# Performance work log

Hardware: AMD Instinct MI355X
Metric: run time of the kernel (lower is better)

Reference implementation:

```python
import jax, jax.numpy as jnp
import numpy as np

N, F, S, D = 8, 16, 196, 1024
H = 8
HD = D // H
L = 1 + F * S  # global feature token + f*s patch tokens


def _ln(x, g, b, eps=1e-5):
    m = x.mean(-1, keepdims=True)
    v = ((x - m) ** 2).mean(-1, keepdims=True)
    return (x - m) / jnp.sqrt(v + eps) * g + b


def _attn(q, k, v, hd):
    s = jnp.einsum('bqd,bkd->bqk', q, k) / jnp.sqrt(jnp.asarray(hd, q.dtype))
    return jnp.einsum('bqk,bkd->bqd', jax.nn.softmax(s, axis=-1), v)


def setup_inputs() -> dict:
    key = jax.random.key(0)
    ks = jax.random.split(key, 8)
    sc = 0.02
    return {
        'x': jax.random.normal(ks[0], (N, L, D), jnp.float32),
        'W_in': jax.random.normal(ks[1], (D, D), jnp.float32) * sc,
        'b_in': jnp.zeros((D,), jnp.float32),
        'g_in': jnp.ones((D,), jnp.float32),
        'beta_in': jnp.zeros((D,), jnp.float32),
        'W_q': jax.random.normal(ks[2], (D, D), jnp.float32) * sc,
        'W_k': jax.random.normal(ks[3], (D, D), jnp.float32) * sc,
        'W_v': jax.random.normal(ks[4], (D, D), jnp.float32) * sc,
        'g_out': jnp.ones((D,), jnp.float32),
        'beta_out': jnp.zeros((D,), jnp.float32),
        'W_out': jax.random.normal(ks[5], (D, D), jnp.float32) * sc,
        'b_out': jnp.zeros((D,), jnp.float32),
        'att_type': 1,  # 1 == 'time', 0 == 'space' (static)
    }


def reference(x, W_in, b_in, g_in, beta_in, W_q, W_k, W_v, g_out, beta_out, W_out, b_out, att_type):
    n = x.shape[0]
    nh = n * H
    # in_fc: Linear + LayerNorm
    x = _ln(x @ W_in + b_in, g_in, beta_in)
    q, k, v = x @ W_q, x @ W_k, x @ W_v

    def split_heads(y):  # [n, L, D] -> [n*h, L, hd]
        return y.reshape(n, L, H, HD).transpose(0, 2, 1, 3).reshape(nh, L, HD)

    q, k, v = map(split_heads, (q, k, v))
    feat_q, q = q[:, :1], q[:, 1:]
    feat_k, k = k[:, :1], k[:, 1:]
    feat_v, v = v[:, :1], v[:, 1:]

    # token_att is computed in the original but never used (dead code):
    # token_att = _attn(feat_q, k, v, HD)

    if att_type == 1:  # time attention: windows of length F per spatial site
        qt = q.reshape(nh, F, S, HD).transpose(0, 2, 1, 3).reshape(nh * S, F, HD)
        kt = k.reshape(nh, F, S, HD).transpose(0, 2, 1, 3).reshape(nh * S, F, HD)
        vt = v.reshape(nh, F, S, HD).transpose(0, 2, 1, 3).reshape(nh * S, F, HD)
        fk = jnp.tile(feat_k, (S, 1, 1))  # torch .repeat(s,1,1)
        fv = jnp.tile(feat_v, (S, 1, 1))
        kk = jnp.concatenate((fk, kt), axis=1)  # [nh*s, 1+f, hd]
        vv = jnp.concatenate((fv, vt), axis=1)
        seq = _attn(qt, kk, vv, HD)  # [nh*s, f, hd]
        seq = seq.reshape(nh, S, F, HD).transpose(0, 2, 1, 3).reshape(nh, F * S, HD)
    else:  # space attention: windows of length S per frame
        qs = q.reshape(nh * F, S, HD)
        ks_ = k.reshape(nh * F, S, HD)
        vs = v.reshape(nh * F, S, HD)
        fk = jnp.tile(feat_k, (F, 1, 1))
        fv = jnp.tile(feat_v, (F, 1, 1))
        kk = jnp.concatenate((fk, ks_), axis=1)  # [nh*f, 1+s, hd]
        vv = jnp.concatenate((fv, vs), axis=1)
        seq = _attn(qs, kk, vv, HD)  # [nh*f, s, hd]
        seq = seq.reshape(nh, F * S, HD)

    out = jnp.concatenate((feat_q, seq), axis=1)  # [nh, L, hd]
    out = out.reshape(n, H, L, HD).transpose(0, 2, 1, 3).reshape(n, L, D)
    out = _ln(out, g_out, beta_out) @ W_out + b_out
    return out
```

## Files before the change

### kernel.cpp

```cpp
#include <hip/hip_runtime.h>
#include <stdint.h>

#define N_B 8
#define F_T 16
#define S_T 196
#define D_M 1024
#define H_N 8
#define HD  128
#define L_T 3137
#define M_R (N_B * L_T)
#define M_P 25216

typedef __attribute__((ext_vector_type(8))) short bf16x8;
typedef __attribute__((ext_vector_type(4))) float f32x4;

__device__ __forceinline__ float b2f(unsigned int u) {
  union { unsigned int i; float f; } x; x.i = u << 16; return x.f;
}
__device__ __forceinline__ unsigned short f2b(float f) {
  union { float f; unsigned int i; } x; x.f = f;
  unsigned int r = x.i + 0x7fffu + ((x.i >> 16) & 1u);
  return (unsigned short)(r >> 16);
}

__global__ __launch_bounds__(256) void convert_pad(const float* __restrict__ x,
                                                   unsigned short* __restrict__ xb,
                                                   int nreal) {
  const int total4 = M_P * 1024 / 4;
  const int stride = gridDim.x * 256;
  for (int i = blockIdx.x * 256 + threadIdx.x; i < total4; i += stride) {
    const int e = i * 4;
    float4 v;
    if (e < nreal) v = *(const float4*)(x + e);
    else { v.x = 0.f; v.y = 0.f; v.z = 0.f; v.w = 0.f; }
    ushort4 o;
    o.x = f2b(v.x); o.y = f2b(v.y); o.z = f2b(v.z); o.w = f2b(v.w);
    *(ushort4*)(xb + e) = o;
  }
}

struct WP { const float* s[5]; unsigned short* d[5]; };
__global__ __launch_bounds__(256) void transpose5(WP p) {
  __shared__ float t[32][33];
  const int w = blockIdx.z;
  const float* W = p.s[w];
  unsigned short* Wt = p.d[w];
  const int tx = threadIdx.x, ty = threadIdx.y;
  const int n0 = blockIdx.x * 32, k0 = blockIdx.y * 32;
#pragma unroll
  for (int i = 0; i < 4; i++)
    t[ty + i * 8][tx] = W[(size_t)(k0 + ty + i * 8) * D_M + n0 + tx];
  __syncthreads();
#pragma unroll
  for (int i = 0; i < 4; i++)
    Wt[(size_t)(n0 + ty + i * 8) * D_M + k0 + tx] = f2b(t[tx][ty + i * 8]);
}

__device__ __forceinline__ void async16(const unsigned short* g, unsigned short* l) {
  __builtin_amdgcn_global_load_lds((const __attribute__((address_space(1))) void*)g,
                                   (__attribute__((address_space(3))) void*)l, 16, 0, 0);
}

struct Outs { void* p[3]; };

#define MFMA_Q(AV, MLO)                                                        \
  __builtin_amdgcn_s_setprio(1);                                               \
  _Pragma("unroll") for (int m_ = 0; m_ < 4; ++m_)                             \
      _Pragma("unroll") for (int n_ = 0; n_ < 4; ++n_)                         \
          acc[(MLO) + m_][n_] = __builtin_amdgcn_mfma_f32_16x16x32_bf16(       \
              AV[(MLO) + m_], bv[n_], acc[(MLO) + m_][n_], 0, 0, 0);           \
  __builtin_amdgcn_s_setprio(0);

#define TILE_ONE(T, BUF, STGB, STGA, VMN)                                      \
  do {                                                                         \
    const unsigned short* Ab = sA + (BUF) * 16384 + aOff;                      \
    const unsigned short* Bb = sB + (BUF) * 16384 + bOff;                      \
    if (STGB) {                                                                \
      async16(gB + ((T) + 1) * 64,          sBst + (1 - (BUF)) * 16384);       \
      async16(gB + ((T) + 1) * 64 + 65536,  sBst + (1 - (BUF)) * 16384 + 4096);\
    }                                                                          \
    _Pragma("unroll") for (int m_ = 0; m_ < 4; ++m_)                           \
        av0[m_] = *(const bf16x8*)(Ab + m_ * 1024 + sl0);                      \
    _Pragma("unroll") for (int n_ = 0; n_ < 4; ++n_)                           \
        bv[n_] = *(const bf16x8*)(Bb + n_ * 1024 + sl0);                       \
    _Pragma("unroll") for (int m_ = 0; m_ < 4; ++m_)                           \
        av1[m_] = *(const bf16x8*)(Ab + m_ * 1024 + sl1);                      \
    MFMA_Q(av0, 0)                                                             \
    if (STGB) {                                                                \
      async16(gB + ((T) + 1) * 64 + 131072, sBst + (1 - (BUF)) * 16384 + 8192);\
      async16(gB + ((T) + 1) * 64 + 196608, sBst + (1 - (BUF)) * 16384 + 12288);\
    }                                                                          \
    _Pragma("unroll") for (int m_ = 0; m_ < 4; ++m_)                           \
        av0[4 + m_] = *(const bf16x8*)(Ab + (4 + m_) * 1024 + sl0);            \
    _Pragma("unroll") for (int m_ = 0; m_ < 4; ++m_)                           \
        av1[4 + m_] = *(const bf16x8*)(Ab + (4 + m_) * 1024 + sl1);            \
    MFMA_Q(av0, 4)                                                             \
    asm volatile("s_waitcnt lgkmcnt(0)" ::: "memory");                         \
    __builtin_amdgcn_s_barrier();                                              \
    asm volatile("" ::: "memory");                                             \
    if (STGA) {                                                                \
      async16(gA + ((T) + 2) * 64,          sAst + (BUF) * 16384);             \
      async16(gA + ((T) + 2) * 64 + 65536,  sAst + (BUF) * 16384 + 4096);      \
    }                                                                          \
    _Pragma("unroll") for (int n_ = 0; n_ < 4; ++n_)                           \
        bv[n_] = *(const bf16x8*)(Bb + n_ * 1024 + sl1);                       \
    MFMA_Q(av1, 0)                                                             \
    if (STGA) {                                                                \
      async16(gA + ((T) + 2) * 64 + 131072, sAst + (BUF) * 16384 + 8192);      \
      async16(gA + ((T) + 2) * 64 + 196608, sAst + (BUF) * 16384 + 12288);     \
    }                                                                          \
    MFMA_Q(av1, 4)                                                             \
    if ((VMN) == 4)                                                            \
      asm volatile("s_waitcnt vmcnt(4) lgkmcnt(0)" ::: "memory");              \
    else if ((VMN) == 0)                                                       \
      asm volatile("s_waitcnt vmcnt(0) lgkmcnt(0)" ::: "memory");              \
    else                                                                       \
      asm volatile("s_waitcnt lgkmcnt(0)" ::: "memory");                       \
    __builtin_amdgcn_s_barrier();                                              \
    asm volatile("" ::: "memory");                                             \
  } while (0)

template <int MODE>
__global__ __launch_bounds__(512, 2) void gemm_bt(const unsigned short* __restrict__ A,
                                                  const unsigned short* __restrict__ Bt,
                                                  const float* __restrict__ bias,
                                                  Outs o, int Mreal) {
  __shared__ __align__(16) unsigned short lds[65536];
  unsigned short* sA = lds;
  unsigned short* sB = lds + 32768;

  const int tid = threadIdx.x;
  const int lane = tid & 63;
  const int wv = tid >> 6;
  const int wm = wv >> 2, wn = wv & 3;
  const int l15 = lane & 15, kg = lane >> 4;

  constexpr int NCT = (MODE == 3) ? 12 : 4;
  constexpr int NWG = 99 * NCT;
  constexpr int Q8 = NWG >> 3, R8 = NWG & 7;
  const int xcd = blockIdx.x & 7, off = blockIdx.x >> 3;
  const int lin = (xcd < R8 ? xcd * (Q8 + 1) : R8 * (Q8 + 1) + (xcd - R8) * Q8) + off;
  const int band = lin / 396;
  const int rem = lin - band * 396;
  const int rowBase = (rem >> 2) * 256;
  const int colBase = (band * 4 + (rem & 3)) * 256;

  const int srow = lane >> 3;
  const int gk = ((lane & 7) ^ srow) * 8;
  const unsigned short* gA = A + (size_t)(rowBase + wv * 8 + srow) * 1024 + gk;
  const unsigned short* gB = Bt + (size_t)(colBase + wv * 8 + srow) * 1024 + gk;
  unsigned short* sAst = sA + wv * 512 + lane * 8;
  unsigned short* sBst = sB + wv * 512 + lane * 8;

  const int aOff = (wm * 128 + l15) * 64;
  const int bOff = (wn * 64 + l15) * 64;
  const int sl0 = ((kg) ^ (l15 & 7)) * 8;
  const int sl1 = ((4 + kg) ^ (l15 & 7)) * 8;

  f32x4 acc[8][4] = {};
  bf16x8 av0[8], av1[8], bv[4];

#pragma unroll
  for (int i = 0; i < 4; i++) async16(gA + i * 65536, sAst + i * 4096);
#pragma unroll
  for (int i = 0; i < 4; i++) async16(gB + i * 65536, sBst + i * 4096);
#pragma unroll
  for (int i = 0; i < 4; i++) async16(gA + i * 65536 + 64, sAst + 16384 + i * 4096);
  asm volatile("s_waitcnt vmcnt(4)" ::: "memory");
  __builtin_amdgcn_s_barrier();
  asm volatile("" ::: "memory");

#pragma unroll 1
  for (int tp = 0; tp < 7; ++tp) {
    const int t0 = tp * 2;
    TILE_ONE(t0, 0, true, true, 4);
    TILE_ONE(t0 + 1, 1, true, true, 4);
  }
  TILE_ONE(14, 0, true, false, 0);
  TILE_ONE(15, 1, false, false, -1);

  __syncthreads();
  if (MODE == 2) {
    float* Cf = (float*)lds;
    float* outF = (float*)o.p[0];
#pragma unroll
    for (int p = 0; p < 2; ++p) {
      if (p) __syncthreads();
      if (wm == p) {
#pragma unroll
        for (int n = 0; n < 4; ++n) {
          const int col_l = wn * 64 + n * 16 + l15;
          const float bval = bias[colBase + col_l];
#pragma unroll
          for (int m = 0; m < 8; ++m)
#pragma unroll
            for (int r = 0; r < 4; ++r)
              Cf[(m * 16 + kg * 4 + r) * 256 + col_l] = acc[m][n][r] + bval;
        }
      }
      __syncthreads();
#pragma unroll
      for (int t2 = 0; t2 < 16; ++t2) {
        const int g = t2 * 512 + tid;
        const int row = g >> 6, ch = g & 63;
        const int grow = rowBase + p * 128 + row;
        if (grow < Mreal)
          *(float4*)(outF + (size_t)grow * 1024 + colBase + ch * 4) =
              *(const float4*)(Cf + row * 256 + ch * 4);
      }
    }
  } else {
    unsigned short* Cs = lds;
#pragma unroll
    for (int n = 0; n < 4; ++n) {
      const int col_l = wn * 64 + n * 16 + l15;
      const float bval = (MODE == 1) ? bias[colBase + col_l] : 0.f;
#pragma unroll
      for (int m = 0; m < 8; ++m)
#pragma unroll
        for (int r = 0; r < 4; ++r)
          Cs[(wm * 128 + m * 16 + kg * 4 + r) * 256 + col_l] = f2b(acc[m][n][r] + bval);
    }
    __syncthreads();
    unsigned short* C;
    int cbase;
    if (MODE == 3) { C = (unsigned short*)o.p[colBase >> 10]; cbase = colBase & 1023; }
    else { C = (unsigned short*)o.p[0]; cbase = colBase; }
#pragma unroll
    for (int t2 = 0; t2 < 16; ++t2) {
      const int g = t2 * 512 + tid;
      const int row = g >> 5, ch = g & 31;
      const int grow = rowBase + row;
      if (grow < Mreal)
        *(uint4*)(C + (size_t)grow * 1024 + cbase + ch * 8) =
            *(const uint4*)(Cs + row * 256 + ch * 8);
    }
  }
}

__global__ __launch_bounds__(256) void ln_kernel(const unsigned short* __restrict__ src,
                                                 const unsigned short* __restrict__ src0,
                                                 const float* __restrict__ g,
                                                 const float* __restrict__ beta,
                                                 unsigned short* __restrict__ out, int Mreal) {
  const int wv = threadIdx.x >> 6, lane = threadIdx.x & 63;
  const int row = blockIdx.x * 4 + wv;
  const int c0 = lane * 8;
  unsigned short* op = out + (size_t)row * 1024 + c0;
  if (row >= Mreal) {
    uint4 z; z.x = 0; z.y = 0; z.z = 0; z.w = 0;
    *(uint4*)op = z; *(uint4*)(op + 512) = z;
    return;
  }
  const unsigned short* s = src;
  if (src0 != nullptr && (row % L_T) == 0) s = src0;
  const unsigned short* ip = s + (size_t)row * 1024 + c0;
  const uint4 ra = *(const uint4*)ip;
  const uint4 rb = *(const uint4*)(ip + 512);
  float xs[16];
  xs[0] = b2f(ra.x & 0xffffu);  xs[1] = b2f(ra.x >> 16);
  xs[2] = b2f(ra.y & 0xffffu);  xs[3] = b2f(ra.y >> 16);
  xs[4] = b2f(ra.z & 0xffffu);  xs[5] = b2f(ra.z >> 16);
  xs[6] = b2f(ra.w & 0xffffu);  xs[7] = b2f(ra.w >> 16);
  xs[8] = b2f(rb.x & 0xffffu);  xs[9] = b2f(rb.x >> 16);
  xs[10] = b2f(rb.y & 0xffffu); xs[11] = b2f(rb.y >> 16);
  xs[12] = b2f(rb.z & 0xffffu); xs[13] = b2f(rb.z >> 16);
  xs[14] = b2f(rb.w & 0xffffu); xs[15] = b2f(rb.w >> 16);
  float sum = 0.f, sq = 0.f;
#pragma unroll
  for (int i = 0; i < 16; ++i) { sum += xs[i]; sq += xs[i] * xs[i]; }
#pragma unroll
  for (int off = 32; off > 0; off >>= 1) {
    sum += __shfl_xor(sum, off);
    sq += __shfl_xor(sq, off);
  }
  const float mean = sum * (1.f / 1024.f);
  const float var = sq * (1.f / 1024.f) - mean * mean;
  const float rstd = rsqrtf(var + 1e-5f);
  const float4 g0 = *(const float4*)(g + c0),        g1 = *(const float4*)(g + c0 + 4);
  const float4 g2 = *(const float4*)(g + c0 + 512),  g3 = *(const float4*)(g + c0 + 516);
  const float4 b0 = *(const float4*)(beta + c0),       b1 = *(const float4*)(beta + c0 + 4);
  const float4 b2 = *(const float4*)(beta + c0 + 512), b3 = *(const float4*)(beta + c0 + 516);
  float gg[16] = {g0.x, g0.y, g0.z, g0.w, g1.x, g1.y, g1.z, g1.w,
                  g2.x, g2.y, g2.z, g2.w, g3.x, g3.y, g3.z, g3.w};
  float bb[16] = {b0.x, b0.y, b0.z, b0.w, b1.x, b1.y, b1.z, b1.w,
                  b2.x, b2.y, b2.z, b2.w, b3.x, b3.y, b3.z, b3.w};
  unsigned short ov[16];
#pragma unroll
  for (int i = 0; i < 16; ++i) ov[i] = f2b((xs[i] - mean) * rstd * gg[i] + bb[i]);
  uint4 wa, wb;
  wa.x = (unsigned)ov[0] | ((unsigned)ov[1] << 16);
  wa.y = (unsigned)ov[2] | ((unsigned)ov[3] << 16);
  wa.z = (unsigned)ov[4] | ((unsigned)ov[5] << 16);
  wa.w = (unsigned)ov[6] | ((unsigned)ov[7] << 16);
  wb.x = (unsigned)ov[8] | ((unsigned)ov[9] << 16);
  wb.y = (unsigned)ov[10] | ((unsigned)ov[11] << 16);
  wb.z = (unsigned)ov[12] | ((unsigned)ov[13] << 16);
  wb.w = (unsigned)ov[14] | ((unsigned)ov[15] << 16);
  *(uint4*)op = wa;
  *(uint4*)(op + 512) = wb;
}

#define ATT_T_BLOCKS (64 * 49)
__global__ __launch_bounds__(256) void attn_kernel(const unsigned short* __restrict__ q,
                                                   const unsigned short* __restrict__ k,
                                                   const unsigned short* __restrict__ v,
                                                   unsigned short* __restrict__ out,
                                                   const int* __restrict__ att_type) {
  __shared__ __align__(16) char smem[22528];
  const int tid = threadIdx.x;
  const int bid = blockIdx.x;
  const int at = att_type[0];

  if (at == 1) {
    if (bid >= ATT_T_BLOCKS) return;
    const int lane = tid & 63, wv = tid >> 6;
    const int l15 = lane & 15, kg = lane >> 4;
    const int hb = bid / 49, sb = bid - hb * 49;
    const int s = sb * 4 + wv;
    const int n = hb >> 3, h = hb & 7;
    const int fi = (hb * S_T + s) & 63;
    const size_t frow = (size_t)(fi >> 3) * L_T;
    const int fcol = (fi & 7) * HD;
    const int qbase = n * L_T + 1 + s;
    const int hcol = h * HD;

    unsigned short* Pl = (unsigned short*)(smem + wv * 5632);
    unsigned short* Vl = (unsigned short*)(smem + wv * 5632 + 1024);

    {
      const int dim0 = l15 * 8;
#pragma unroll
      for (int p = 0; p < 5; p++) {
        const int key = p * 4 + kg;
        if (key < 17) {
          const unsigned short* vp = (key == 0)
              ? (v + frow * 1024 + fcol + dim0)
              : (v + (size_t)(qbase + (key - 1) * S_T) * 1024 + hcol + dim0);
          uint4 r = *(const uint4*)vp;
          unsigned int* wp = (unsigned int*)Vl + key * 65 + l15 * 4;
          wp[0] = r.x; wp[1] = r.y; wp[2] = r.z; wp[3] = r.w;
        }
      }
    }

    bf16x8 aq[4], bk0[4], bk1[4];
    {
      const unsigned short* qp = q + (size_t)(qbase + l15 * S_T) * 1024 + hcol + kg * 8;
      const unsigned short* kp = (l15 == 0)
          ? (k + frow * 1024 + fcol + kg * 8)
          : (k + (size_t)(qbase + (l15 - 1) * S_T) * 1024 + hcol + kg * 8);
      const unsigned short* kp1 = k + (size_t)(qbase + 15 * S_T) * 1024 + hcol + kg * 8;
#pragma unroll
      for (int t = 0; t < 4; t++) {
        aq[t] = *(const bf16x8*)(qp + t * 32);
        bk0[t] = *(const bf16x8*)(kp + t * 32);
        if (l15 == 0) bk1[t] = *(const bf16x8*)(kp1 + t * 32);
        else {
          bf16x8 z = {};
          bk1[t] = z;
        }
      }
    }

    f32x4 c0 = {}, c1 = {};
#pragma unroll
    for (int t = 0; t < 4; t++) {
      c0 = __builtin_amdgcn_mfma_f32_16x16x32_bf16(aq[t], bk0[t], c0, 0, 0, 0);
      c1 = __builtin_amdgcn_mfma_f32_16x16x32_bf16(aq[t], bk1[t], c1, 0, 0, 0);
    }

    const float scl = 0.08838834764831845f;
#pragma unroll
    for (int r = 0; r < 4; r++) {
      float v0 = c0[r] * scl;
      float k16 = __shfl(c1[r] * scl, lane & 48);
      float mx = v0;
#pragma unroll
      for (int m = 1; m < 16; m <<= 1) mx = fmaxf(mx, __shfl_xor(mx, m));
      mx = fmaxf(mx, k16);
      float p = __expf(v0 - mx);
      float p16 = __expf(k16 - mx);
      float sum = p;
#pragma unroll
      for (int m = 1; m < 16; m <<= 1) sum += __shfl_xor(sum, m);
      sum += p16;
      const float inv = 1.f / sum;
      const int row = kg * 4 + r;
      Pl[row * 32 + l15] = f2b(p * inv);
      Pl[row * 32 + 16 + l15] = (l15 == 0) ? f2b(p16 * inv) : (unsigned short)0;
    }

    bf16x8 ap = *(const bf16x8*)(Pl + l15 * 32 + kg * 8);
    f32x4 oo[8];
#pragma unroll
    for (int nt = 0; nt < 8; nt++) {
      const int dim = nt * 16 + l15;
      bf16x8 bvv;
#pragma unroll
      for (int j = 0; j < 8; j++) {
        const int key = kg * 8 + j;
        const int kc = (key < 17) ? key : 0;
        bvv[j] = (short)Vl[kc * 130 + dim];
      }
      f32x4 z = {};
      oo[nt] = __builtin_amdgcn_mfma_f32_16x16x32_bf16(ap, bvv, z, 0, 0, 0);
    }

#pragma unroll
    for (int nt = 0; nt < 8; nt++)
#pragma unroll
      for (int r = 0; r < 4; r++)
        Vl[(kg * 4 + r) * 130 + nt * 16 + l15] = f2b(oo[nt][r]);
#pragma unroll
    for (int t = 0; t < 4; t++) {
      const int row = t * 4 + kg;
      uint4 w = *(const uint4*)(Vl + row * 130 + l15 * 8);
      *(uint4*)(out + (size_t)(qbase + row * S_T) * 1024 + hcol + l15 * 8) = w;
    }
    return;
  }

  float (*qs)[132] = (float (*)[132])smem;
  float (*sc)[212] = (float (*)[212])(smem + 8448);
  const int hb = bid / 208;
  const int rem = bid - hb * 208;
  const int f = rem / 13, qc = rem - f * 13;
  const int n = hb >> 3, h = hb & 7;
  const int fi = (hb * F_T + f) & 63;
  const size_t frow = (size_t)(fi >> 3) * L_T;
  const int fcol = (fi & 7) * HD;
  const int kbase = n * L_T + 1 + f * S_T;
  const int qbase = kbase + qc * 16;
  const int nk = S_T + 1;
  const int nqv = (qc == 12) ? 4 : 16;
  const int hcol = h * HD;

  {
    const int i = tid >> 4, db = (tid & 15) * 8;
    float* dst = &qs[i][db];
    if (i < nqv) {
      const unsigned short* qp = q + (size_t)(qbase + i) * 1024 + hcol + db;
      uint4 r = *(const uint4*)qp;
      dst[0] = b2f(r.x & 0xffffu); dst[1] = b2f(r.x >> 16);
      dst[2] = b2f(r.y & 0xffffu); dst[3] = b2f(r.y >> 16);
      dst[4] = b2f(r.z & 0xffffu); dst[5] = b2f(r.z >> 16);
      dst[6] = b2f(r.w & 0xffffu); dst[7] = b2f(r.w >> 16);
    } else {
#pragma unroll
      for (int u = 0; u < 8; u++) dst[u] = 0.f;
    }
  }
  __syncthreads();

  const int nslot = 16 * nk;
  for (int slot = tid; slot < nslot; slot += 256) {
    const int i = slot / nk, j = slot - i * nk;
    const unsigned short* kp = (j == 0)
        ? (k + frow * 1024 + fcol)
        : (k + (size_t)(kbase + (j - 1)) * 1024 + hcol);
    float acc = 0.f;
#pragma unroll 4
    for (int d = 0; d < 128; d += 8) {
      uint4 r = *(const uint4*)(kp + d);
      acc += qs[i][d + 0] * b2f(r.x & 0xffffu);
      acc += qs[i][d + 1] * b2f(r.x >> 16);
      acc += qs[i][d + 2] * b2f(r.y & 0xffffu);
      acc += qs[i][d + 3] * b2f(r.y >> 16);
      acc += qs[i][d + 4] * b2f(r.z & 0xffffu);
      acc += qs[i][d + 5] * b2f(r.z >> 16);
      acc += qs[i][d + 6] * b2f(r.w & 0xffffu);
      acc += qs[i][d + 7] * b2f(r.w >> 16);
    }
    sc[i][j] = acc * 0.08838834764831845f;
  }
  __syncthreads();

  if (tid < 16) {
    const int i = tid;
    float m = -1e30f;
    for (int j = 0; j < nk; j++) m = fmaxf(m, sc[i][j]);
    float ssum = 0.f;
    for (int j = 0; j < nk; j++) {
      float e = __expf(sc[i][j] - m);
      sc[i][j] = e;
      ssum += e;
    }
    const float inv = 1.f / ssum;
    for (int j = 0; j < nk; j++) sc[i][j] *= inv;
  }
  __syncthreads();

  {
    const int i = tid >> 4, db = (tid & 15) * 8;
    float o[8];
#pragma unroll
    for (int u = 0; u < 8; u++) o[u] = 0.f;
    for (int j = 0; j < nk; j++) {
      const unsigned short* vp = (j == 0)
          ? (v + frow * 1024 + fcol + db)
          : (v + (size_t)(kbase + (j - 1)) * 1024 + hcol + db);
      const float p = sc[i][j];
      uint4 r = *(const uint4*)vp;
      o[0] += p * b2f(r.x & 0xffffu); o[1] += p * b2f(r.x >> 16);
      o[2] += p * b2f(r.y & 0xffffu); o[3] += p * b2f(r.y >> 16);
      o[4] += p * b2f(r.z & 0xffffu); o[5] += p * b2f(r.z >> 16);
      o[6] += p * b2f(r.w & 0xffffu); o[7] += p * b2f(r.w >> 16);
    }
    if (i < nqv) {
      unsigned short* op = out + (size_t)(qbase + i) * 1024 + hcol + db;
      uint4 w;
      w.x = (unsigned)f2b(o[0]) | ((unsigned)f2b(o[1]) << 16);
      w.y = (unsigned)f2b(o[2]) | ((unsigned)f2b(o[3]) << 16);
      w.z = (unsigned)f2b(o[4]) | ((unsigned)f2b(o[5]) << 16);
      w.w = (unsigned)f2b(o[6]) | ((unsigned)f2b(o[7]) << 16);
      *(uint4*)op = w;
    }
  }
}

extern "C" void kernel_launch(void* const* d_in, const int* in_sizes, int n_in,
                              void* d_out, int out_size, void* d_ws, size_t ws_size,
                              hipStream_t stream) {
  const float* x        = (const float*)d_in[0];
  const float* W_in     = (const float*)d_in[1];
  const float* b_in     = (const float*)d_in[2];
  const float* g_in     = (const float*)d_in[3];
  const float* beta_in  = (const float*)d_in[4];
  const float* W_q      = (const float*)d_in[5];
  const float* W_k      = (const float*)d_in[6];
  const float* W_v      = (const float*)d_in[7];
  const float* g_out    = (const float*)d_in[8];
  const float* beta_out = (const float*)d_in[9];
  const float* W_out    = (const float*)d_in[10];
  const float* b_out    = (const float*)d_in[11];
  const int* att_type   = (const int*)d_in[12];
  float* out = (float*)d_out;

  char* ws = (char*)d_ws;
  const size_t MB = (size_t)M_P * 1024 * 2;
  unsigned short* xb = (unsigned short*)(ws + 0 * MB);
  unsigned short* t1 = (unsigned short*)(ws + 1 * MB);
  unsigned short* xh = (unsigned short*)(ws + 2 * MB);
  unsigned short* kb = (unsigned short*)(ws + 3 * MB);
  unsigned short* vb = (unsigned short*)(ws + 4 * MB);
  unsigned short* wt = (unsigned short*)(ws + 5 * MB);
  const size_t WSZ = (size_t)1024 * 1024;
  unsigned short* wt_in  = wt;
  unsigned short* wqkv   = wt + 1 * WSZ;
  unsigned short* wt_out = wt + 4 * WSZ;

  convert_pad<<<2048, 256, 0, stream>>>(x, xb, M_R * 1024);

  WP wp;
  wp.s[0] = W_in; wp.s[1] = W_q; wp.s[2] = W_k; wp.s[3] = W_v; wp.s[4] = W_out;
  wp.d[0] = wt_in;
  wp.d[1] = wqkv;
  wp.d[2] = wqkv + 1 * WSZ;
  wp.d[3] = wqkv + 2 * WSZ;
  wp.d[4] = wt_out;
  transpose5<<<dim3(32, 32, 5), dim3(32, 8), 0, stream>>>(wp);

  Outs o1; o1.p[0] = t1; o1.p[1] = nullptr; o1.p[2] = nullptr;
  gemm_bt<1><<<396, 512, 0, stream>>>(xb, wt_in, b_in, o1, M_P);
  ln_kernel<<<M_P / 4, 256, 0, stream>>>(t1, nullptr, g_in, beta_in, xh, M_R);

  Outs oq; oq.p[0] = t1; oq.p[1] = kb; oq.p[2] = vb;
  gemm_bt<3><<<1188, 512, 0, stream>>>(xh, wqkv, nullptr, oq, M_P);

  attn_kernel<<<13312, 256, 0, stream>>>(t1, kb, vb, xb, att_type);
  ln_kernel<<<M_P / 4, 256, 0, stream>>>(xb, t1, g_out, beta_out, xh, M_R);

  Outs oo; oo.p[0] = out; oo.p[1] = nullptr; oo.p[2] = nullptr;
  gemm_bt<2><<<396, 512, 0, stream>>>(xh, wt_out, b_out, oo, M_R);
}
```

Measured before the change: 548.7 us.

## Fold LayerNorms into GEMM epilogues via weight scaling and row statistics

Removes both standalone LayerNorm kernels. LayerNorm gamma is folded into the transposed weights, and precomputed column sums (u = g·W, w = beta·W) let the following GEMM apply mean/rstd correction in its epilogue. Row sum and sum-of-squares are accumulated with atomics in the producing GEMM or attention epilogues. This saves two full read/write passes over the activation, at the cost of atomics, an extra small stats kernel, and numerical risk from the E[x²]-mean² variance formula on un-normalized bf16 inputs.

```diff
diff --git a/kernel.cpp b/kernel.cpp
--- a/kernel.cpp
+++ b/kernel.cpp
@@ -10,6 +10,7 @@
 #define L_T 3137
 #define M_R (N_B * L_T)
 #define M_P 25216
+#define M_T 25344
 
 typedef __attribute__((ext_vector_type(8))) short bf16x8;
 typedef __attribute__((ext_vector_type(4))) float f32x4;
@@ -39,21 +40,56 @@
   }
 }
 
-struct WP { const float* s[5]; unsigned short* d[5]; };
+struct WP { const float* s[5]; unsigned short* d[5]; const float* g[5]; };
 __global__ __launch_bounds__(256) void transpose5(WP p) {
   __shared__ float t[32][33];
   const int w = blockIdx.z;
   const float* W = p.s[w];
   unsigned short* Wt = p.d[w];
+  const float* gsp = p.g[w];
   const int tx = threadIdx.x, ty = threadIdx.y;
   const int n0 = blockIdx.x * 32, k0 = blockIdx.y * 32;
 #pragma unroll
   for (int i = 0; i < 4; i++)
     t[ty + i * 8][tx] = W[(size_t)(k0 + ty + i * 8) * D_M + n0 + tx];
   __syncthreads();
+  const float gs = gsp ? gsp[k0 + tx] : 1.f;
 #pragma unroll
   for (int i = 0; i < 4; i++)
-    Wt[(size_t)(n0 + ty + i * 8) * D_M + k0 + tx] = f2b(t[tx][ty + i * 8]);
+    Wt[(size_t)(n0 + ty + i * 8) * D_M + k0 + tx] = f2b(t[tx][ty + i * 8] * gs);
+}
+
+__global__ __launch_bounds__(256) void ustats(const float* __restrict__ Wq,
+                                              const float* __restrict__ Wk,
+                                              const float* __restrict__ Wv,
+                                              const float* __restrict__ Wo,
+                                              const float* __restrict__ g_in,
+                                              const float* __restrict__ beta_in,
+                                              const float* __restrict__ g_out,
+                                              const float* __restrict__ beta_out,
+                                              const float* __restrict__ b_out,
+                                              float* __restrict__ uvec,
+                                              float* __restrict__ wvec) {
+  const int jb = blockIdx.x >> 4;
+  const int chunk = blockIdx.x & 15;
+  const int j = jb * 256 + threadIdx.x;
+  const float* W; const float* g; const float* be; int col;
+  if (j < 3072) {
+    const int wsel = j >> 10;
+    W = (wsel == 0) ? Wq : ((wsel == 1) ? Wk : Wv);
+    col = j & 1023; g = g_in; be = beta_in;
+  } else {
+    W = Wo; col = j - 3072; g = g_out; be = beta_out;
+  }
+  float au = 0.f, aw = 0.f;
+  const int k0 = chunk * 64;
+  for (int k = k0; k < k0 + 64; ++k) {
+    const float wv_ = W[(size_t)k * 1024 + col];
+    au += g[k] * wv_; aw += be[k] * wv_;
+  }
+  if (chunk == 0 && j >= 3072) aw += b_out[col];
+  atomicAdd(&uvec[j], au);
+  atomicAdd(&wvec[j], aw);
 }
 
 __device__ __forceinline__ void async16(const unsigned short* g, unsigned short* l) {
@@ -124,7 +160,11 @@
 __global__ __launch_bounds__(512, 2) void gemm_bt(const unsigned short* __restrict__ A,
                                                   const unsigned short* __restrict__ Bt,
                                                   const float* __restrict__ bias,
-                                                  Outs o, int Mreal) {
+                                                  Outs o, int Mreal,
+                                                  float* __restrict__ st1,
+                                                  float* __restrict__ st2,
+                                                  const float* __restrict__ uvec,
+                                                  const float* __restrict__ wvec) {
   __shared__ __align__(16) unsigned short lds[65536];
   unsigned short* sA = lds;
   unsigned short* sB = lds + 32768;
@@ -183,20 +223,30 @@
   if (MODE == 2) {
     float* Cf = (float*)lds;
     float* outF = (float*)o.p[0];
+    float uu[4], ww[4];
+#pragma unroll
+    for (int n = 0; n < 4; ++n) {
+      const int c = colBase + wn * 64 + n * 16 + l15;
+      uu[n] = uvec[c]; ww[n] = wvec[c];
+    }
 #pragma unroll
     for (int p = 0; p < 2; ++p) {
       if (p) __syncthreads();
       if (wm == p) {
 #pragma unroll
-        for (int n = 0; n < 4; ++n) {
-          const int col_l = wn * 64 + n * 16 + l15;
-          const float bval = bias[colBase + col_l];
-#pragma unroll
-          for (int m = 0; m < 8; ++m)
-#pragma unroll
-            for (int r = 0; r < 4; ++r)
-              Cf[(m * 16 + kg * 4 + r) * 256 + col_l] = acc[m][n][r] + bval;
-        }
+        for (int m = 0; m < 8; ++m)
+#pragma unroll
+          for (int r = 0; r < 4; ++r) {
+            const int lrow = m * 16 + kg * 4 + r;
+            const int grow = rowBase + p * 128 + lrow;
+            const float2 st = *(const float2*)(st2 + (size_t)grow * 2);
+            const float mu = st.x * (1.f / 1024.f);
+            const float rstd = rsqrtf(st.y * (1.f / 1024.f) - mu * mu + 1e-5f);
+#pragma unroll
+            for (int n = 0; n < 4; ++n)
+              Cf[lrow * 256 + wn * 64 + n * 16 + l15] =
+                  rstd * (acc[m][n][r] - mu * uu[n]) + ww[n];
+          }
       }
       __syncthreads();
 #pragma unroll
@@ -209,23 +259,86 @@
               *(const float4*)(Cf + row * 256 + ch * 4);
       }
     }
+  } else if (MODE == 1) {
+    unsigned short* Cs = lds;
+    float bvals[4];
+#pragma unroll
+    for (int n = 0; n < 4; ++n) bvals[n] = bias[colBase + wn * 64 + n * 16 + l15];
+#pragma unroll
+    for (int m = 0; m < 8; ++m)
+#pragma unroll
+      for (int r = 0; r < 4; ++r) {
+        const int lrow = wm * 128 + m * 16 + kg * 4 + r;
+        float s = 0.f, sq = 0.f;
+#pragma unroll
+        for (int n = 0; n < 4; ++n) {
+          const float v = acc[m][n][r] + bvals[n];
+          Cs[lrow * 256 + wn * 64 + n * 16 + l15] = f2b(v);
+          s += v; sq += v * v;
+        }
+        s += __shfl_xor(s, 1); sq += __shfl_xor(sq, 1);
+        s += __shfl_xor(s, 2); sq += __shfl_xor(sq, 2);
+        s += __shfl_xor(s, 4); sq += __shfl_xor(sq, 4);
+        s += __shfl_xor(s, 8); sq += __shfl_xor(sq, 8);
+        if (l15 == 0) {
+          const int grow = rowBase + lrow;
+          atomicAdd(&st1[(size_t)grow * 2], s);
+          atomicAdd(&st1[(size_t)grow * 2 + 1], sq);
+        }
+      }
+    __syncthreads();
+    unsigned short* C = (unsigned short*)o.p[0];
+#pragma unroll
+    for (int t2 = 0; t2 < 16; ++t2) {
+      const int g = t2 * 512 + tid;
+      const int row = g >> 5, ch = g & 31;
+      const int grow = rowBase + row;
+      if (grow < Mreal)
+        *(uint4*)(C + (size_t)grow * 1024 + colBase + ch * 8) =
+            *(const uint4*)(Cs + row * 256 + ch * 8);
+    }
   } else {
     unsigned short* Cs = lds;
+    float uu[4], ww[4];
 #pragma unroll
     for (int n = 0; n < 4; ++n) {
-      const int col_l = wn * 64 + n * 16 + l15;
-      const float bval = (MODE == 1) ? bias[colBase + col_l] : 0.f;
-#pragma unroll
-      for (int m = 0; m < 8; ++m)
-#pragma unroll
-        for (int r = 0; r < 4; ++r)
-          Cs[(wm * 128 + m * 16 + kg * 4 + r) * 256 + col_l] = f2b(acc[m][n][r] + bval);
-    }
+      const int c = colBase + wn * 64 + n * 16 + l15;
+      uu[n] = uvec[c]; ww[n] = wvec[c];
+    }
+    const int r0m = rowBase % L_T;
+    const int flocal = (r0m == 0) ? 0 : (L_T - r0m);
+    const bool qtile = (colBase < 1024);
+#pragma unroll
+    for (int m = 0; m < 8; ++m)
+#pragma unroll
+      for (int r = 0; r < 4; ++r) {
+        const int lrow = wm * 128 + m * 16 + kg * 4 + r;
+        const int grow = rowBase + lrow;
+        const float2 st = *(const float2*)(st1 + (size_t)grow * 2);
+        const float mu = st.x * (1.f / 1024.f);
+        const float rstd = rsqrtf(st.y * (1.f / 1024.f) - mu * mu + 1e-5f);
+        float vv[4];
+#pragma unroll
+        for (int n = 0; n < 4; ++n) {
+          vv[n] = rstd * (acc[m][n][r] - mu * uu[n]) + ww[n];
+          Cs[lrow * 256 + wn * 64 + n * 16 + l15] = f2b(vv[n]);
+        }
+        if (qtile && lrow == flocal) {
+          float s = vv[0] + vv[1] + vv[2] + vv[3];
+          float sq = vv[0] * vv[0] + vv[1] * vv[1] + vv[2] * vv[2] + vv[3] * vv[3];
+          s += __shfl_xor(s, 1); sq += __shfl_xor(sq, 1);
+          s += __shfl_xor(s, 2); sq += __shfl_xor(sq, 2);
+          s += __shfl_xor(s, 4); sq += __shfl_xor(sq, 4);
+          s += __shfl_xor(s, 8); sq += __shfl_xor(sq, 8);
+          if (l15 == 0) {
+            atomicAdd(&st2[(size_t)grow * 2], s);
+            atomicAdd(&st2[(size_t)grow * 2 + 1], sq);
+          }
+        }
+      }
     __syncthreads();
-    unsigned short* C;
-    int cbase;
-    if (MODE == 3) { C = (unsigned short*)o.p[colBase >> 10]; cbase = colBase & 1023; }
-    else { C = (unsigned short*)o.p[0]; cbase = colBase; }
+    unsigned short* C = (unsigned short*)o.p[colBase >> 10];
+    const int cbase = colBase & 1023;
 #pragma unroll
     for (int t2 = 0; t2 < 16; ++t2) {
       const int g = t2 * 512 + tid;
@@ -238,79 +351,22 @@
   }
 }
 
-__global__ __launch_bounds__(256) void ln_kernel(const unsigned short* __restrict__ src,
-                                                 const unsigned short* __restrict__ src0,
-                                                 const float* __restrict__ g,
-                                                 const float* __restrict__ beta,
-                                                 unsigned short* __restrict__ out, int Mreal) {
-  const int wv = threadIdx.x >> 6, lane = threadIdx.x & 63;
-  const int row = blockIdx.x * 4 + wv;
-  const int c0 = lane * 8;
-  unsigned short* op = out + (size_t)row * 1024 + c0;
-  if (row >= Mreal) {
-    uint4 z; z.x = 0; z.y = 0; z.z = 0; z.w = 0;
-    *(uint4*)op = z; *(uint4*)(op + 512) = z;
-    return;
-  }
-  const unsigned short* s = src;
-  if (src0 != nullptr && (row % L_T) == 0) s = src0;
-  const unsigned short* ip = s + (size_t)row * 1024 + c0;
-  const uint4 ra = *(const uint4*)ip;
-  const uint4 rb = *(const uint4*)(ip + 512);
-  float xs[16];
-  xs[0] = b2f(ra.x & 0xffffu);  xs[1] = b2f(ra.x >> 16);
-  xs[2] = b2f(ra.y & 0xffffu);  xs[3] = b2f(ra.y >> 16);
-  xs[4] = b2f(ra.z & 0xffffu);  xs[5] = b2f(ra.z >> 16);
-  xs[6] = b2f(ra.w & 0xffffu);  xs[7] = b2f(ra.w >> 16);
-  xs[8] = b2f(rb.x & 0xffffu);  xs[9] = b2f(rb.x >> 16);
-  xs[10] = b2f(rb.y & 0xffffu); xs[11] = b2f(rb.y >> 16);
-  xs[12] = b2f(rb.z & 0xffffu); xs[13] = b2f(rb.z >> 16);
-  xs[14] = b2f(rb.w & 0xffffu); xs[15] = b2f(rb.w >> 16);
-  float sum = 0.f, sq = 0.f;
-#pragma unroll
-  for (int i = 0; i < 16; ++i) { sum += xs[i]; sq += xs[i] * xs[i]; }
-#pragma unroll
-  for (int off = 32; off > 0; off >>= 1) {
-    sum += __shfl_xor(sum, off);
-    sq += __shfl_xor(sq, off);
-  }
-  const float mean = sum * (1.f / 1024.f);
-  const float var = sq * (1.f / 1024.f) - mean * mean;
-  const float rstd = rsqrtf(var + 1e-5f);
-  const float4 g0 = *(const float4*)(g + c0),        g1 = *(const float4*)(g + c0 + 4);
-  const float4 g2 = *(const float4*)(g + c0 + 512),  g3 = *(const float4*)(g + c0 + 516);
-  const float4 b0 = *(const float4*)(beta + c0),       b1 = *(const float4*)(beta + c0 + 4);
-  const float4 b2 = *(const float4*)(beta + c0 + 512), b3 = *(const float4*)(beta + c0 + 516);
-  float gg[16] = {g0.x, g0.y, g0.z, g0.w, g1.x, g1.y, g1.z, g1.w,
-                  g2.x, g2.y, g2.z, g2.w, g3.x, g3.y, g3.z, g3.w};
-  float bb[16] = {b0.x, b0.y, b0.z, b0.w, b1.x, b1.y, b1.z, b1.w,
-                  b2.x, b2.y, b2.z, b2.w, b3.x, b3.y, b3.z, b3.w};
-  unsigned short ov[16];
-#pragma unroll
-  for (int i = 0; i < 16; ++i) ov[i] = f2b((xs[i] - mean) * rstd * gg[i] + bb[i]);
-  uint4 wa, wb;
-  wa.x = (unsigned)ov[0] | ((unsigned)ov[1] << 16);
-  wa.y = (unsigned)ov[2] | ((unsigned)ov[3] << 16);
-  wa.z = (unsigned)ov[4] | ((unsigned)ov[5] << 16);
-  wa.w = (unsigned)ov[6] | ((unsigned)ov[7] << 16);
-  wb.x = (unsigned)ov[8] | ((unsigned)ov[9] << 16);
-  wb.y = (unsigned)ov[10] | ((unsigned)ov[11] << 16);
-  wb.z = (unsigned)ov[12] | ((unsigned)ov[13] << 16);
-  wb.w = (unsigned)ov[14] | ((unsigned)ov[15] << 16);
-  *(uint4*)op = wa;
-  *(uint4*)(op + 512) = wb;
-}
-
 #define ATT_T_BLOCKS (64 * 49)
 __global__ __launch_bounds__(256) void attn_kernel(const unsigned short* __restrict__ q,
                                                    const unsigned short* __restrict__ k,
                                                    const unsigned short* __restrict__ v,
                                                    unsigned short* __restrict__ out,
-                                                   const int* __restrict__ att_type) {
+                                                   const int* __restrict__ att_type,
+                                                   float* __restrict__ st2) {
   __shared__ __align__(16) char smem[22528];
   const int tid = threadIdx.x;
   const int bid = blockIdx.x;
   const int at = att_type[0];
+
+  if (bid < N_B) {
+    const size_t ro = (size_t)bid * L_T * 1024;
+    *(uint2*)(out + ro + tid * 4) = *(const uint2*)(q + ro + tid * 4);
+  }
 
   if (at == 1) {
     if (bid >= ATT_T_BLOCKS) return;
@@ -405,6 +461,22 @@
       }
       f32x4 z = {};
       oo[nt] = __builtin_amdgcn_mfma_f32_16x16x32_bf16(ap, bvv, z, 0, 0, 0);
+    }
+
+#pragma unroll
+    for (int r = 0; r < 4; r++) {
+      float s = 0.f, sq = 0.f;
+#pragma unroll
+      for (int nt = 0; nt < 8; nt++) { const float vv = oo[nt][r]; s += vv; sq += vv * vv; }
+      s += __shfl_xor(s, 1); sq += __shfl_xor(sq, 1);
+      s += __shfl_xor(s, 2); sq += __shfl_xor(sq, 2);
+      s += __shfl_xor(s, 4); sq += __shfl_xor(sq, 4);
+      s += __shfl_xor(s, 8); sq += __shfl_xor(sq, 8);
+      if (l15 == 0) {
+        const size_t grow = (size_t)(qbase + (kg * 4 + r) * S_T);
+        atomicAdd(&st2[grow * 2], s);
+        atomicAdd(&st2[grow * 2 + 1], sq);
+      }
     }
 
 #pragma unroll
@@ -516,6 +588,18 @@
       w.w = (unsigned)f2b(o[6]) | ((unsigned)f2b(o[7]) << 16);
       *(uint4*)op = w;
     }
+    float s = 0.f, sq = 0.f;
+#pragma unroll
+    for (int u = 0; u < 8; u++) { s += o[u]; sq += o[u] * o[u]; }
+    s += __shfl_xor(s, 1); sq += __shfl_xor(sq, 1);
+    s += __shfl_xor(s, 2); sq += __shfl_xor(sq, 2);
+    s += __shfl_xor(s, 4); sq += __shfl_xor(sq, 4);
+    s += __shfl_xor(s, 8); sq += __shfl_xor(sq, 8);
+    if ((tid & 15) == 0 && i < nqv) {
+      const size_t grow = (size_t)(qbase + i);
+      atomicAdd(&st2[grow * 2], s);
+      atomicAdd(&st2[grow * 2 + 1], sq);
+    }
   }
 }
 
@@ -549,6 +633,12 @@
   unsigned short* wt_in  = wt;
   unsigned short* wqkv   = wt + 1 * WSZ;
   unsigned short* wt_out = wt + 4 * WSZ;
+  float* stats1 = (float*)(ws + 5 * MB + 5 * WSZ * sizeof(unsigned short));
+  float* stats2 = stats1 + 2 * M_T;
+  float* uvec   = stats2 + 2 * M_T;
+  float* wvec   = uvec + 4096;
+
+  hipMemsetAsync(stats1, 0, (size_t)(2 * M_T * 2 + 4096 * 2) * sizeof(float), stream);
 
   convert_pad<<<2048, 256, 0, stream>>>(x, xb, M_R * 1024);
 
@@ -559,18 +649,23 @@
   wp.d[2] = wqkv + 1 * WSZ;
   wp.d[3] = wqkv + 2 * WSZ;
   wp.d[4] = wt_out;
+  wp.g[0] = nullptr; wp.g[1] = g_in; wp.g[2] = g_in; wp.g[3] = g_in; wp.g[4] = g_out;
   transpose5<<<dim3(32, 32, 5), dim3(32, 8), 0, stream>>>(wp);
 
+  ustats<<<256, 256, 0, stream>>>(W_q, W_k, W_v, W_out, g_in, beta_in, g_out, beta_out,
+                                  b_out, uvec, wvec);
+
   Outs o1; o1.p[0] = t1; o1.p[1] = nullptr; o1.p[2] = nullptr;
-  gemm_bt<1><<<396, 512, 0, stream>>>(xb, wt_in, b_in, o1, M_P);
-  ln_kernel<<<M_P / 4, 256, 0, stream>>>(t1, nullptr, g_in, beta_in, xh, M_R);
-
-  Outs oq; oq.p[0] = t1; oq.p[1] = kb; oq.p[2] = vb;
-  gemm_bt<3><<<1188, 512, 0, stream>>>(xh, wqkv, nullptr, oq, M_P);
-
-  attn_kernel<<<13312, 256, 0, stream>>>(t1, kb, vb, xb, att_type);
-  ln_kernel<<<M_P / 4, 256, 0, stream>>>(xb, t1, g_out, beta_out, xh, M_R);
+  gemm_bt<1><<<396, 512, 0, stream>>>(xb, wt_in, b_in, o1, M_P, stats1, nullptr,
+                                      nullptr, nullptr);
+
+  Outs oq; oq.p[0] = xh; oq.p[1] = kb; oq.p[2] = vb;
+  gemm_bt<3><<<1188, 512, 0, stream>>>(t1, wqkv, nullptr, oq, M_P, stats1, stats2,
+                                       uvec, wvec);
+
+  attn_kernel<<<13312, 256, 0, stream>>>(xh, kb, vb, xb, att_type, stats2);
 
   Outs oo; oo.p[0] = out; oo.p[1] = nullptr; oo.p[2] = nullptr;
-  gemm_bt<2><<<396, 512, 0, stream>>>(xh, wt_out, b_out, oo, M_R);
-}
+  gemm_bt<2><<<396, 512, 0, stream>>>(xb, wt_out, nullptr, oo, M_R, nullptr, stats2,
+                                      uvec + 3072, wvec + 3072);
+}
```

Measured after the change: 647.4 us. 18.0% more time.
